# Kernel tuning notes

Measured on AMD Instinct MI355X. Metric: run time of the kernel, lower is better.

## Reference

```python
import jax, jax.numpy as jnp
import numpy as np

EMBED_DIM = 1024
NUM_HEADS = 16
HEAD_DIM = EMBED_DIM // NUM_HEADS


def setup_inputs() -> dict:
    key = jax.random.key(0)
    k_x, k_wqkv, k_bqkv, k_wout, k_bout = jax.random.split(key, 5)
    s = 1.0 / np.sqrt(EMBED_DIM)
    return {
        "x": jax.random.normal(k_x, (2, 2048, EMBED_DIM), dtype=jnp.float32),
        "w_qkv": jax.random.uniform(k_wqkv, (EMBED_DIM, 3 * EMBED_DIM), jnp.float32, -s, s),
        "b_qkv": jax.random.uniform(k_bqkv, (3 * EMBED_DIM,), jnp.float32, -s, s),
        "w_out": jax.random.uniform(k_wout, (EMBED_DIM, EMBED_DIM), jnp.float32, -s, s),
        "b_out": jax.random.uniform(k_bout, (EMBED_DIM,), jnp.float32, -s, s),
    }


def reference(x, w_qkv, b_qkv, w_out, b_out):
    B, S, D = x.shape
    H, Hd = NUM_HEADS, HEAD_DIM
    # qkv projection, then per-head chunk: layout matches torch view(B,S,H,3*Hd).chunk(3,-1)
    qkv = (x @ w_qkv + b_qkv).reshape(B, S, H, 3, Hd)  # [B,S,H,3,Hd]
    q = qkv[..., 0, :]  # [B,S,H,Hd]
    k = qkv[..., 1, :]
    v = qkv[..., 2, :]
    scale = 1.0 / np.sqrt(Hd).astype(np.float32)
    scores = jnp.einsum("bqhd,bkhd->bhqk", q, k) * scale  # [B,H,S,S]
    probs = jax.nn.softmax(scores, axis=-1)
    out = jnp.einsum("bhqk,bkhd->bqhd", probs, v).reshape(B, S, D)
    return out @ w_out + b_out
```

## Files before the change

kernel.cpp:

```cpp
#include <hip/hip_runtime.h>
#include <hip/hip_bf16.h>


typedef __bf16 bf16;
typedef __bf16 bf16x8 __attribute__((ext_vector_type(8)));
typedef float  f32x4  __attribute__((ext_vector_type(4)));
typedef float  f32x16 __attribute__((ext_vector_type(16)));
typedef unsigned int uint;
typedef unsigned int uint2v __attribute__((ext_vector_type(2)));

__device__ __forceinline__ void gload_lds16(const void* g, void* l) {
  __builtin_amdgcn_global_load_lds(
      (const __attribute__((address_space(1))) unsigned int*)g,
      (__attribute__((address_space(3))) unsigned int*)l, 16, 0, 0);
}

__device__ __forceinline__ uint pkbf16(float lo, float hi) {
  union { bf16 h[2]; uint u; } t;
  t.h[0] = (bf16)lo; t.h[1] = (bf16)hi;
  return t.u;
}

__device__ __forceinline__ void pl32swapu(uint& a, uint& b) {
  uint2v r = __builtin_amdgcn_permlane32_swap(a, b, false, false);
  a = r.x; b = r.y;
}
__device__ __forceinline__ void pl32swapf(float& a, float& b) {
  uint ua = __builtin_bit_cast(uint, a), ub = __builtin_bit_cast(uint, b);
  pl32swapu(ua, ub);
  a = __builtin_bit_cast(float, ua); b = __builtin_bit_cast(float, ub);
}

__global__ __launch_bounds__(256) void k_convert(const float* __restrict__ in,
                                                 bf16* __restrict__ out, int n) {
  int i = (blockIdx.x * blockDim.x + threadIdx.x) * 8;
  if (i >= n) return;
  float4 a = *(const float4*)(in + i);
  float4 b = *(const float4*)(in + i + 4);
  bf16x8 o;
  o[0] = (bf16)a.x; o[1] = (bf16)a.y; o[2] = (bf16)a.z; o[3] = (bf16)a.w;
  o[4] = (bf16)b.x; o[5] = (bf16)b.y; o[6] = (bf16)b.z; o[7] = (bf16)b.w;
  *(bf16x8*)(out + i) = o;
}

template<bool PERM>
__global__ __launch_bounds__(256) void k_transpose(const float* __restrict__ in,
                                                   bf16* __restrict__ out, int K, int N) {
  __shared__ float tile[32][33];
  int n0 = blockIdx.x * 32, k0 = blockIdx.y * 32;
  int tx = threadIdx.x, ty = threadIdx.y;
#pragma unroll
  for (int i = 0; i < 4; i++)
    tile[ty + i * 8][tx] = in[(size_t)(k0 + ty + i * 8) * N + n0 + tx];
  __syncthreads();
#pragma unroll
  for (int i = 0; i < 4; i++) {
    int n = n0 + ty + i * 8;
    int row = n;
    if (PERM) {
      int rem = n % 192;
      row = (rem >> 6) * 1024 + (n / 192) * 64 + (rem & 63);
    }
    out[(size_t)row * K + k0 + tx] = (bf16)tile[tx][ty + i * 8];
  }
}

template<int BM, int BN>
__device__ __forceinline__ void gemm_tile(const bf16* __restrict__ A, const bf16* __restrict__ B,
                                          int K, int m0, int n0,
                                          bf16* As, bf16* Bs, f32x4 acc[BM / 32][BN / 32]) {
  const int tid  = threadIdx.x;
  const int lane = tid & 63;
  const int wr   = (tid >> 7) & 1;
  const int wc   = (tid >> 6) & 1;
  constexpr int LA = BM / 64, LB = BN / 64;
  auto stage = [&](int k0v, int b) {
#pragma unroll
    for (int i = 0; i < LA; i++) {
      int row = i * 64 + (tid >> 2);
      int sw  = (tid & 3) ^ (row & 3);
      gload_lds16(A + (size_t)(m0 + row) * K + k0v + sw * 8, (char*)As + b * (BM * 64) + i * 4096 + tid * 16);
    }
#pragma unroll
    for (int i = 0; i < LB; i++) {
      int row = i * 64 + (tid >> 2);
      int sw  = (tid & 3) ^ (row & 3);
      gload_lds16(B + (size_t)(n0 + row) * K + k0v + sw * 8, (char*)Bs + b * (BN * 64) + i * 4096 + tid * 16);
    }
  };
  const int nk = K / 32;
  stage(0, 0); stage(32, 1); stage(64, 2);
  for (int t = 0; t < nk; t++) {
    if (t < nk - 2) {
      if constexpr (LA + LB == 4) asm volatile("s_waitcnt vmcnt(8)" ::: "memory");
      else                        asm volatile("s_waitcnt vmcnt(6)" ::: "memory");
    } else if (t < nk - 1) {
      if constexpr (LA + LB == 4) asm volatile("s_waitcnt vmcnt(4)" ::: "memory");
      else                        asm volatile("s_waitcnt vmcnt(3)" ::: "memory");
    } else {
      asm volatile("s_waitcnt vmcnt(0)" ::: "memory");
    }
    __builtin_amdgcn_s_barrier();
    asm volatile("" ::: "memory");
    if (t + 3 < nk) stage((t + 3) * 32, (t + 3) & 3);
    const int cur = t & 3;
    bf16x8 af[BM / 32], bfr[BN / 32];
#pragma unroll
    for (int r = 0; r < BM / 32; r++) {
      int ra = wr * (BM / 2) + r * 16 + (lane & 15);
      af[r]  = *(const bf16x8*)((const char*)As + cur * (BM * 64) + ra * 64 + ((((lane >> 4) << 4)) ^ ((ra & 3) << 4)));
    }
#pragma unroll
    for (int c = 0; c < BN / 32; c++) {
      int rb = wc * (BN / 2) + c * 16 + (lane & 15);
      bfr[c] = *(const bf16x8*)((const char*)Bs + cur * (BN * 64) + rb * 64 + ((((lane >> 4) << 4)) ^ ((rb & 3) << 4)));
    }
#pragma unroll
    for (int r = 0; r < BM / 32; r++)
#pragma unroll
      for (int c = 0; c < BN / 32; c++)
        acc[r][c] = __builtin_amdgcn_mfma_f32_16x16x32_bf16(af[r], bfr[c], acc[r][c], 0, 0, 0);
    asm volatile("" ::: "memory");
  }
}

__global__ __launch_bounds__(512, 2) void k_gemm_qkv(const bf16* __restrict__ A, const bf16* __restrict__ Bt,
                                                     const float* __restrict__ bias,
                                                     bf16* __restrict__ qb, bf16* __restrict__ kb,
                                                     bf16* __restrict__ vtb) {
  __shared__ char GS[131072];
  const int tid  = threadIdx.x;
  const int lane = tid & 63;
  const int wave = tid >> 6;
  const int wr   = wave >> 2;
  const int wc   = wave & 3;
  const int m0 = blockIdx.x * 256, n0 = blockIdx.y * 256;
  const int K = 1024;

  f32x4 acc[8][4];
  f32x4 zero = {0.f, 0.f, 0.f, 0.f};
#pragma unroll
  for (int ms = 0; ms < 8; ms++)
#pragma unroll
    for (int ns = 0; ns < 4; ns++) acc[ms][ns] = zero;

  const int ccs = tid & 7;
  int rA[2], rB[2];
  {
    int lr0 = tid >> 3;
    rA[0] = lr0;
    rB[0] = (lr0 & 31) + ((lr0 >> 5) << 6);
    int lr1 = 64 + lr0;
    rA[1] = (lr1 & 63) + 128;
    rB[1] = (lr1 & 31) + ((lr1 >> 5) << 6);
  }
  const bf16* Agp[2]; const bf16* Bgp[2];
  int Alo[2], Blo[2];
#pragma unroll
  for (int j = 0; j < 2; j++) {
    Agp[j] = A  + (size_t)(m0 + rA[j]) * K + (ccs ^ (rA[j] & 7)) * 8;
    Alo[j] = rA[j] * 128 + ccs * 16;
    Bgp[j] = Bt + (size_t)(n0 + rB[j]) * K + (ccs ^ (rB[j] & 7)) * 8;
    Blo[j] = rB[j] * 128 + ccs * 16;
  }
  auto stA = [&](int t, int h) {
    int b = t & 1;
#pragma unroll
    for (int j = 0; j < 2; j++)
      gload_lds16(Agp[j] + (size_t)(h * 64) * K + t * 64, GS + b * 32768 + Alo[j] + h * 8192);
  };
  auto stB = [&](int t, int h) {
    int b = t & 1;
#pragma unroll
    for (int j = 0; j < 2; j++)
      gload_lds16(Bgp[j] + (size_t)(h * 32) * K + t * 64, GS + 65536 + b * 32768 + Blo[j] + h * 4096);
  };

  bf16x8 af[4][2], bf0[2][2], bf1[2][2];
  auto rdA = [&](const char* Ab, int mh) {
#pragma unroll
    for (int ms = 0; ms < 4; ms++)
#pragma unroll
      for (int ks = 0; ks < 2; ks++) {
        int row = wr * 128 + (mh * 4 + ms) * 16 + (lane & 15);
        int ch = (ks * 4 + (lane >> 4)) ^ (row & 7);
        af[ms][ks] = *(const bf16x8*)(Ab + row * 128 + ch * 16);
      }
  };
  auto rdB = [&](const char* Bb, int nh, bf16x8 (&bfx)[2][2]) {
#pragma unroll
    for (int ns = 0; ns < 2; ns++)
#pragma unroll
      for (int ks = 0; ks < 2; ks++) {
        int row = wc * 64 + (nh * 2 + ns) * 16 + (lane & 15);
        int ch = (ks * 4 + (lane >> 4)) ^ (row & 7);
        bfx[ns][ks] = *(const bf16x8*)(Bb + row * 128 + ch * 16);
      }
  };
  auto mm = [&](int mh, int nh, bf16x8 (&bfx)[2][2]) {
    __builtin_amdgcn_s_setprio(1);
#pragma unroll
    for (int ks = 0; ks < 2; ks++)
#pragma unroll
      for (int ms = 0; ms < 4; ms++)
#pragma unroll
        for (int ns = 0; ns < 2; ns++)
          acc[mh * 4 + ms][nh * 2 + ns] =
              __builtin_amdgcn_mfma_f32_16x16x32_bf16(af[ms][ks], bfx[ns][ks],
                                                      acc[mh * 4 + ms][nh * 2 + ns], 0, 0, 0);
    __builtin_amdgcn_s_setprio(0);
  };

#define BARRIER do { asm volatile("" ::: "memory"); __builtin_amdgcn_s_barrier(); \
                     asm volatile("" ::: "memory"); } while (0)

  stA(0, 0); stB(0, 0); stB(0, 1); stA(0, 1);
  stA(1, 0); stB(1, 0); stB(1, 1);
  asm volatile("s_waitcnt vmcnt(6)" ::: "memory");
  __builtin_amdgcn_s_barrier();
  asm volatile("" ::: "memory");

  for (int I = 0; I < 8; I++) {
    const int T = 2 * I;
    const char* Ab0 = GS;
    const char* Bb0 = GS + 65536;
    const char* Ab1 = GS + 32768;
    const char* Bb1 = GS + 65536 + 32768;
    const bool m2 = (T + 2 < 16), m3 = (T + 3 < 16);

    rdA(Ab0, 0); rdB(Bb0, 0, bf0);
    stA(T + 1, 1);
    BARRIER;
    mm(0, 0, bf0);

    rdB(Bb0, 1, bf1);
    if (m2) stA(T + 2, 0);
    BARRIER;
    mm(0, 1, bf1);

    rdA(Ab0, 1);
    if (m2) stB(T + 2, 0);
    BARRIER;
    mm(1, 0, bf0);

    if (m2) {
      stB(T + 2, 1);
      asm volatile("s_waitcnt vmcnt(6)" ::: "memory");
    } else {
      asm volatile("s_waitcnt vmcnt(0)" ::: "memory");
    }
    __builtin_amdgcn_s_barrier();
    asm volatile("" ::: "memory");
    mm(1, 1, bf1);

    rdA(Ab1, 0); rdB(Bb1, 0, bf0);
    if (m2) stA(T + 2, 1);
    BARRIER;
    mm(0, 0, bf0);

    rdB(Bb1, 1, bf1);
    if (m3) stA(T + 3, 0);
    BARRIER;
    mm(0, 1, bf1);

    rdA(Ab1, 1);
    if (m3) stB(T + 3, 0);
    BARRIER;
    mm(1, 0, bf0);

    if (m3) {
      stB(T + 3, 1);
      asm volatile("s_waitcnt vmcnt(6)" ::: "memory");
    } else {
      asm volatile("s_waitcnt vmcnt(0)" ::: "memory");
    }
    __builtin_amdgcn_s_barrier();
    asm volatile("" ::: "memory");
    mm(1, 1, bf1);
  }
#undef BARRIER

  const int group = n0 >> 10;
  const int hb = (n0 & 1023) >> 6;
  const int b_ = m0 >> 11;
  const float QSs = 0.125f * 1.4426950408889634f;
  char* TL = GS;

  if (group < 2) {
#pragma unroll
    for (int ms = 0; ms < 8; ms++) {
      int mloc = wr * 128 + ms * 16 + ((lane >> 4) << 2);
#pragma unroll
      for (int ns = 0; ns < 4; ns++) {
        int nloc = wc * 64 + ns * 16 + (lane & 15);
        int np = n0 + nloc;
        float bv = bias[((np & 1023) >> 6) * 192 + group * 64 + (np & 63)];
#pragma unroll
        for (int g = 0; g < 4; g++) {
          float v = acc[ms][ns][g] + bv;
          if (group == 0) v *= QSs;
          int m = mloc + g;
          int byte = m * 512 + ((((nloc >> 3) ^ (m & 7)) << 4) | ((nloc & 7) << 1));
          *(bf16*)(TL + byte) = (bf16)v;
        }
      }
    }
    __syncthreads();
    bf16* dst = (group == 0) ? qb : kb;
#pragma unroll
    for (int it = 0; it < 16; it++) {
      int cid = it * 512 + tid;
      int row = cid >> 5, cc = cid & 31;
      int hh = hb + (cc >> 3), ck = cc & 7;
      bf16x8 v8 = *(const bf16x8*)(TL + row * 512 + ((cc ^ (row & 7)) << 4));
      *(bf16x8*)(dst + ((size_t)(b_ * 16 + hh) * 2048 + (m0 & 2047) + row) * 64 + ck * 8) = v8;
    }
  } else {
#pragma unroll
    for (int ms = 0; ms < 8; ms++) {
      int mloc = wr * 128 + ms * 16 + ((lane >> 4) << 2);
#pragma unroll
      for (int ns = 0; ns < 4; ns++) {
        int nloc = wc * 64 + ns * 16 + (lane & 15);
        int np = n0 + nloc;
        float bv = bias[((np & 1023) >> 6) * 192 + 2 * 64 + (np & 63)];
#pragma unroll
        for (int g = 0; g < 4; g++) {
          float v = acc[ms][ns][g] + bv;
          int m = mloc + g;
          int byte = nloc * 512 + ((((m >> 3) ^ (nloc & 7)) << 4) | ((m & 7) << 1));
          *(bf16*)(TL + byte) = (bf16)v;
        }
      }
    }
    __syncthreads();
#pragma unroll
    for (int it = 0; it < 16; it++) {
      int cid = it * 512 + tid;
      int row = cid >> 5, mc = cid & 31;
      int hh = hb + (row >> 6), dd = row & 63;
      bf16x8 v8 = *(const bf16x8*)(TL + row * 512 + ((mc ^ (row & 7)) << 4));
      *(bf16x8*)(vtb + ((size_t)(b_ * 16 + hh) * 64 + dd) * 2048 + (m0 & 2047) + mc * 8) = v8;
    }
  }
}

__global__ __launch_bounds__(256) void k_gemm_out(const bf16* __restrict__ A, const bf16* __restrict__ Bt,
                                                  const float* __restrict__ bias,
                                                  float* __restrict__ out) {
  __shared__ bf16 As[4 * 64 * 32];
  __shared__ bf16 Bs[4 * 128 * 32];
  int m0 = blockIdx.x * 64, n0 = blockIdx.y * 128;
  f32x4 zero = {0.f, 0.f, 0.f, 0.f};
  f32x4 acc[2][4];
#pragma unroll
  for (int r = 0; r < 2; r++)
#pragma unroll
    for (int c = 0; c < 4; c++) acc[r][c] = zero;
  gemm_tile<64, 128>(A, Bt, 1024, m0, n0, As, Bs, acc);
  const int lane = threadIdx.x & 63;
  const int wr = (threadIdx.x >> 7) & 1, wc = (threadIdx.x >> 6) & 1;
#pragma unroll
  for (int r = 0; r < 2; r++) {
    int mbase = m0 + wr * 32 + r * 16 + ((lane >> 4) << 2);
#pragma unroll
    for (int c = 0; c < 4; c++) {
      int n = n0 + wc * 64 + c * 16 + (lane & 15);
      float bv = bias[n];
#pragma unroll
      for (int g = 0; g < 4; g++)
        out[(size_t)(mbase + g) * 1024 + n] = acc[r][c][g] + bv;
    }
  }
}

__global__ __launch_bounds__(512, 4) void k_attn(const bf16* __restrict__ qb, const bf16* __restrict__ kb,
                                                 const bf16* __restrict__ vtb, bf16* __restrict__ ob) {
  __shared__ char SMEM[73728];
  const int tid  = threadIdx.x;
  const int lane = tid & 63;
  const int wave = tid >> 6;
  const int qsub = wave & 3;
  const int half = wave >> 2;
  const int ln31 = lane & 31;
  const int g    = lane >> 5;

  int l = blockIdx.x;
  int x = l & 7, j = l >> 3;
  int qt = j & 15;
  int bh = x * 4 + (j >> 4);

  const int q0 = qt * 128 + qsub * 32;

  bf16x8 qf[4];
  {
    const bf16* qp = qb + ((size_t)bh * 2048 + q0 + ln31) * 64 + g * 8;
#pragma unroll
    for (int dc = 0; dc < 4; dc++) qf[dc] = *(const bf16x8*)(qp + dc * 16);
  }

  const f32x16 z16 = 0.f;
  f32x16 O0 = 0.f, O1 = 0.f;
  float lacc[4] = {0.f, 0.f, 0.f, 0.f};

  const int rbo = ln31 * 144 + (g << 4);
  const char* kbs0 = SMEM + half * 9216 + rbo;
  const char* kbs1 = SMEM + 36864 + half * 9216 + rbo;
  const char* vbs0 = SMEM + 18432 + half * 9216 + rbo;
  const char* vbs1 = SMEM + 36864 + 18432 + half * 9216 + rbo;

  const int c1 = tid, r1 = c1 / 9, cc1 = c1 % 9;
  const int of1 = (cc1 == 8 ? 0 : cc1) * 8;
  const bf16* kg0a = kb  + ((size_t)bh * 2048 +        r1) * 64 + of1;
  const bf16* kg1a = kb  + ((size_t)bh * 2048 + 1024 + r1) * 64 + of1;
  const bf16* vg0a = vtb + ((size_t)bh * 64 + r1) * 2048 +        of1;
  const bf16* vg1a = vtb + ((size_t)bh * 64 + r1) * 2048 + 1024 + of1;
  const int se = tid >> 6;
  const int ce = 512 + (tid & 63), re = ce / 9, cce = ce % 9;
  const int ofe = (cce == 8 ? 0 : cce) * 8;
  const bf16* gext =
      (se == 0) ? kb  + ((size_t)bh * 2048 +        re) * 64 + ofe :
      (se == 1) ? kb  + ((size_t)bh * 2048 + 1024 + re) * 64 + ofe :
      (se == 2) ? vtb + ((size_t)bh * 64 + re) * 2048 +        ofe :
                  vtb + ((size_t)bh * 64 + re) * 2048 + 1024 + ofe;
  const size_t gadv = (se < 2) ? 4096 : 64;
  const int eoff = se * 9216 + ce * 16;

  auto stage = [&](int t, int s) {
    char* bs = SMEM + s * 36864;
    gload_lds16(kg0a + (size_t)t * 4096, bs +         c1 * 16);
    gload_lds16(kg1a + (size_t)t * 4096, bs + 9216  + c1 * 16);
    gload_lds16(vg0a + t * 64,           bs + 18432 + c1 * 16);
    gload_lds16(vg1a + t * 64,           bs + 27648 + c1 * 16);
    if (tid < 256) gload_lds16(gext + (size_t)t * gadv, bs + eoff);
  };

  auto smx = [&](f32x16& sv, bf16x8& f0, bf16x8& f1) {
#pragma unroll
    for (int r = 0; r < 16; r++) sv[r] = __builtin_amdgcn_exp2f(sv[r]);
#pragma unroll
    for (int r = 0; r < 4; r++)
      lacc[r] += (sv[r] + sv[r + 4]) + (sv[r + 8] + sv[r + 12]);
    uint a0 = pkbf16(sv[0], sv[1]), a1 = pkbf16(sv[2], sv[3]);
    uint a2 = pkbf16(sv[4], sv[5]), a3 = pkbf16(sv[6], sv[7]);
    pl32swapu(a0, a2); pl32swapu(a1, a3);
    union { uint w[4]; bf16x8 v; } pa;
    pa.w[0] = a0; pa.w[1] = a1; pa.w[2] = a2; pa.w[3] = a3;
    f0 = pa.v;
    uint b0 = pkbf16(sv[8], sv[9]),  b1 = pkbf16(sv[10], sv[11]);
    uint b2 = pkbf16(sv[12], sv[13]), b3 = pkbf16(sv[14], sv[15]);
    pl32swapu(b0, b2); pl32swapu(b1, b3);
    union { uint w[4]; bf16x8 v; } pb;
    pb.w[0] = b0; pb.w[1] = b1; pb.w[2] = b2; pb.w[3] = b3;
    f1 = pb.v;
  };

  stage(0, 0);
  for (int t = 0; t < 16; t++) {
    asm volatile("s_waitcnt vmcnt(0)" ::: "memory");
    __builtin_amdgcn_s_barrier();
    asm volatile("" ::: "memory");
    if (t + 1 < 16) stage(t + 1, (t + 1) & 1);

    const char* Kb = (t & 1) ? kbs1 : kbs0;
    const char* Vb = (t & 1) ? vbs1 : vbs0;

    f32x16 sA, sB;
    __builtin_amdgcn_s_setprio(1);
    sA = __builtin_amdgcn_mfma_f32_32x32x16_bf16(*(const bf16x8*)(Kb +    0), qf[0], z16, 0, 0, 0);
    sB = __builtin_amdgcn_mfma_f32_32x32x16_bf16(*(const bf16x8*)(Kb + 4608), qf[0], z16, 0, 0, 0);
#pragma unroll
    for (int dc = 1; dc < 4; dc++) {
      sA = __builtin_amdgcn_mfma_f32_32x32x16_bf16(*(const bf16x8*)(Kb + dc * 32),        qf[dc], sA, 0, 0, 0);
      sB = __builtin_amdgcn_mfma_f32_32x32x16_bf16(*(const bf16x8*)(Kb + 4608 + dc * 32), qf[dc], sB, 0, 0, 0);
    }
    __builtin_amdgcn_s_setprio(0);

    bf16x8 fA0, fA1, fB0, fB1;
    smx(sA, fA0, fA1);
    __builtin_amdgcn_s_setprio(1);
    O0 = __builtin_amdgcn_mfma_f32_32x32x16_bf16(*(const bf16x8*)(Vb +    0), fA0, O0, 0, 0, 0);
    O1 = __builtin_amdgcn_mfma_f32_32x32x16_bf16(*(const bf16x8*)(Vb + 4608), fA0, O1, 0, 0, 0);
    O0 = __builtin_amdgcn_mfma_f32_32x32x16_bf16(*(const bf16x8*)(Vb +   32), fA1, O0, 0, 0, 0);
    O1 = __builtin_amdgcn_mfma_f32_32x32x16_bf16(*(const bf16x8*)(Vb + 4640), fA1, O1, 0, 0, 0);
    __builtin_amdgcn_s_setprio(0);
    smx(sB, fB0, fB1);
    __builtin_amdgcn_s_setprio(1);
    O0 = __builtin_amdgcn_mfma_f32_32x32x16_bf16(*(const bf16x8*)(Vb +   64), fB0, O0, 0, 0, 0);
    O1 = __builtin_amdgcn_mfma_f32_32x32x16_bf16(*(const bf16x8*)(Vb + 4672), fB0, O1, 0, 0, 0);
    O0 = __builtin_amdgcn_mfma_f32_32x32x16_bf16(*(const bf16x8*)(Vb +   96), fB1, O0, 0, 0, 0);
    O1 = __builtin_amdgcn_mfma_f32_32x32x16_bf16(*(const bf16x8*)(Vb + 4704), fB1, O1, 0, 0, 0);
    __builtin_amdgcn_s_setprio(0);
    asm volatile("" ::: "memory");
  }

  float l_r = (lacc[0] + lacc[1]) + (lacc[2] + lacc[3]);
  { float o = l_r; pl32swapf(l_r, o); l_r += o; }

  float* Opart = (float*)SMEM;
  float* Ls    = (float*)(SMEM + 36864);
  __syncthreads();
  if (half == 1) {
    float* my = Opart + (qsub * 64 + lane) * 36;
#pragma unroll
    for (int c = 0; c < 4; c++) {
      f32x4 a = {O0[c * 4], O0[c * 4 + 1], O0[c * 4 + 2], O0[c * 4 + 3]};
      f32x4 b = {O1[c * 4], O1[c * 4 + 1], O1[c * 4 + 2], O1[c * 4 + 3]};
      *(f32x4*)(my + c * 4) = a;
      *(f32x4*)(my + 16 + c * 4) = b;
    }
    if (lane < 32) Ls[qsub * 32 + ln31] = l_r;
  }
  __syncthreads();
  bf16 (*Os)[32][72] = reinterpret_cast<bf16 (*)[32][72]>(SMEM + 40960);
  if (half == 0) {
    const float* pr = Opart + (qsub * 64 + lane) * 36;
#pragma unroll
    for (int c = 0; c < 4; c++) {
      f32x4 a = *(const f32x4*)(pr + c * 4);
      f32x4 b = *(const f32x4*)(pr + 16 + c * 4);
#pragma unroll
      for (int k = 0; k < 4; k++) { O0[c * 4 + k] += a[k]; O1[c * 4 + k] += b[k]; }
    }
    l_r += Ls[qsub * 32 + ln31];
    float inv = 1.0f / l_r;
#pragma unroll
    for (int r = 0; r < 16; r++) {
      int d0 = (r & 3) + 8 * (r >> 2) + 4 * g;
      Os[qsub][ln31][d0]      = (bf16)(O0[r] * inv);
      Os[qsub][ln31][d0 + 32] = (bf16)(O1[r] * inv);
    }
  }
  __syncthreads();
  if (half == 0) {
    int b_ = bh >> 4, h = bh & 15;
#pragma unroll
    for (int it = 0; it < 4; it++) {
      int cid = it * 64 + lane;
      int row = cid >> 3, c = cid & 7;
      bf16x8 v8o = *(const bf16x8*)&Os[qsub][row][c * 8];
      *(bf16x8*)(ob + ((size_t)(b_ * 2048 + q0 + row)) * 1024 + h * 64 + c * 8) = v8o;
    }
  }
}

extern "C" void kernel_launch(void* const* d_in, const int* in_sizes, int n_in,
                              void* d_out, int out_size, void* d_ws, size_t ws_size,
                              hipStream_t stream) {
  const float* x     = (const float*)d_in[0];
  const float* w_qkv = (const float*)d_in[1];
  const float* b_qkv = (const float*)d_in[2];
  const float* w_out = (const float*)d_in[3];
  const float* b_out = (const float*)d_in[4];
  float* out = (float*)d_out;

  char* ws = (char*)d_ws;
  bf16* xb  = (bf16*)ws;
  bf16* wqT = (bf16*)(ws + (8ull  << 20));
  bf16* woT = (bf16*)(ws + (14ull << 20));
  bf16* qb  = (bf16*)(ws + (16ull << 20));
  bf16* kb  = (bf16*)(ws + (24ull << 20));
  bf16* vtb = (bf16*)(ws + (32ull << 20));

  k_convert<<<2048, 256, 0, stream>>>(x, xb, 4194304);
  k_transpose<true><<<dim3(96, 32), dim3(32, 8), 0, stream>>>(w_qkv, wqT, 1024, 3072);
  k_transpose<false><<<dim3(32, 32), dim3(32, 8), 0, stream>>>(w_out, woT, 1024, 1024);
  k_gemm_qkv<<<dim3(16, 12), 512, 0, stream>>>(xb, wqT, b_qkv, qb, kb, vtb);
  k_attn<<<512, 512, 0, stream>>>(qb, kb, vtb, xb);
  k_gemm_out<<<dim3(64, 8), 256, 0, stream>>>(xb, woT, b_out, out);
}
```

Measured before the change: 112.4 us.

## Process two 32-row query tiles per wave in attention and fuse prep kernels

The attention kernel now gives each wave 64 query rows (two 32-row MFMA tiles) instead of 32. Each K and V fragment read from LDS is reused across both tiles, and the grid halves to 256 blocks. The three preprocessing kernels (x conversion and two weight transposes) are merged into one launch to cut launch overhead. The cost is more accumulator registers (launch bound lowered to 2 blocks per SM) and fewer blocks, which may leave compute units idle on a 256-CU device.

```diff
diff --git a/kernel.cpp b/kernel.cpp
--- a/kernel.cpp
+++ b/kernel.cpp
@@ -31,24 +31,34 @@
   a = __builtin_bit_cast(float, ua); b = __builtin_bit_cast(float, ub);
 }
 
-__global__ __launch_bounds__(256) void k_convert(const float* __restrict__ in,
-                                                 bf16* __restrict__ out, int n) {
-  int i = (blockIdx.x * blockDim.x + threadIdx.x) * 8;
-  if (i >= n) return;
-  float4 a = *(const float4*)(in + i);
-  float4 b = *(const float4*)(in + i + 4);
-  bf16x8 o;
-  o[0] = (bf16)a.x; o[1] = (bf16)a.y; o[2] = (bf16)a.z; o[3] = (bf16)a.w;
-  o[4] = (bf16)b.x; o[5] = (bf16)b.y; o[6] = (bf16)b.z; o[7] = (bf16)b.w;
-  *(bf16x8*)(out + i) = o;
-}
-
-template<bool PERM>
-__global__ __launch_bounds__(256) void k_transpose(const float* __restrict__ in,
-                                                   bf16* __restrict__ out, int K, int N) {
+__global__ __launch_bounds__(256) void k_prep(const float* __restrict__ x,
+                                              const float* __restrict__ w_qkv,
+                                              const float* __restrict__ w_out,
+                                              bf16* __restrict__ xb,
+                                              bf16* __restrict__ wqT,
+                                              bf16* __restrict__ woT) {
   __shared__ float tile[32][33];
-  int n0 = blockIdx.x * 32, k0 = blockIdx.y * 32;
-  int tx = threadIdx.x, ty = threadIdx.y;
+  const int b = blockIdx.x;
+  const int tid = threadIdx.x;
+  if (b < 2048) {
+    int i = (b * 256 + tid) * 8;
+    float4 a = *(const float4*)(x + i);
+    float4 c = *(const float4*)(x + i + 4);
+    bf16x8 o;
+    o[0] = (bf16)a.x; o[1] = (bf16)a.y; o[2] = (bf16)a.z; o[3] = (bf16)a.w;
+    o[4] = (bf16)c.x; o[5] = (bf16)c.y; o[6] = (bf16)c.z; o[7] = (bf16)c.w;
+    *(bf16x8*)(xb + i) = o;
+    return;
+  }
+  const bool perm = (b < 5120);
+  const float* in = perm ? w_qkv : w_out;
+  bf16* out = perm ? wqT : woT;
+  const int N = perm ? 3072 : 1024;
+  int idx = perm ? (b - 2048) : (b - 5120);
+  int gx = perm ? (idx % 96) : (idx % 32);
+  int gy = perm ? (idx / 96) : (idx / 32);
+  int n0 = gx * 32, k0 = gy * 32;
+  int tx = tid & 31, ty = tid >> 5;
 #pragma unroll
   for (int i = 0; i < 4; i++)
     tile[ty + i * 8][tx] = in[(size_t)(k0 + ty + i * 8) * N + n0 + tx];
@@ -57,11 +67,11 @@
   for (int i = 0; i < 4; i++) {
     int n = n0 + ty + i * 8;
     int row = n;
-    if (PERM) {
+    if (perm) {
       int rem = n % 192;
       row = (rem >> 6) * 1024 + (n / 192) * 64 + (rem & 63);
     }
-    out[(size_t)row * K + k0 + tx] = (bf16)tile[tx][ty + i * 8];
+    out[(size_t)row * 1024 + k0 + tx] = (bf16)tile[tx][ty + i * 8];
   }
 }
 
@@ -374,34 +384,39 @@
   }
 }
 
-__global__ __launch_bounds__(512, 4) void k_attn(const bf16* __restrict__ qb, const bf16* __restrict__ kb,
+__global__ __launch_bounds__(512, 2) void k_attn(const bf16* __restrict__ qb, const bf16* __restrict__ kb,
                                                  const bf16* __restrict__ vtb, bf16* __restrict__ ob) {
   __shared__ char SMEM[73728];
   const int tid  = threadIdx.x;
   const int lane = tid & 63;
   const int wave = tid >> 6;
-  const int qsub = wave & 3;
+  const int qp   = wave & 3;
   const int half = wave >> 2;
   const int ln31 = lane & 31;
   const int g    = lane >> 5;
 
   int l = blockIdx.x;
   int x = l & 7, j = l >> 3;
-  int qt = j & 15;
-  int bh = x * 4 + (j >> 4);
-
-  const int q0 = qt * 128 + qsub * 32;
-
-  bf16x8 qf[4];
+  int qt = j & 7;
+  int bh = x * 4 + (j >> 3);
+
+  const int q0 = qt * 256 + qp * 64;
+
+  bf16x8 qfa[4], qfb[4];
   {
-    const bf16* qp = qb + ((size_t)bh * 2048 + q0 + ln31) * 64 + g * 8;
-#pragma unroll
-    for (int dc = 0; dc < 4; dc++) qf[dc] = *(const bf16x8*)(qp + dc * 16);
+    const bf16* qpa = qb + ((size_t)bh * 2048 + q0 + ln31) * 64 + g * 8;
+    const bf16* qpb = qb + ((size_t)bh * 2048 + q0 + 32 + ln31) * 64 + g * 8;
+#pragma unroll
+    for (int dc = 0; dc < 4; dc++) {
+      qfa[dc] = *(const bf16x8*)(qpa + dc * 16);
+      qfb[dc] = *(const bf16x8*)(qpb + dc * 16);
+    }
   }
 
   const f32x16 z16 = 0.f;
-  f32x16 O0 = 0.f, O1 = 0.f;
-  float lacc[4] = {0.f, 0.f, 0.f, 0.f};
+  f32x16 Oa0 = 0.f, Oa1 = 0.f, Ob0 = 0.f, Ob1 = 0.f;
+  float lacc_a[4] = {0.f, 0.f, 0.f, 0.f};
+  float lacc_b[4] = {0.f, 0.f, 0.f, 0.f};
 
   const int rbo = ln31 * 144 + (g << 4);
   const char* kbs0 = SMEM + half * 9216 + rbo;
@@ -435,12 +450,12 @@
     if (tid < 256) gload_lds16(gext + (size_t)t * gadv, bs + eoff);
   };
 
-  auto smx = [&](f32x16& sv, bf16x8& f0, bf16x8& f1) {
+  auto smx = [&](f32x16& sv, bf16x8& f0, bf16x8& f1, float (&lc)[4]) {
 #pragma unroll
     for (int r = 0; r < 16; r++) sv[r] = __builtin_amdgcn_exp2f(sv[r]);
 #pragma unroll
     for (int r = 0; r < 4; r++)
-      lacc[r] += (sv[r] + sv[r + 4]) + (sv[r + 8] + sv[r + 12]);
+      lc[r] += (sv[r] + sv[r + 4]) + (sv[r + 8] + sv[r + 12]);
     uint a0 = pkbf16(sv[0], sv[1]), a1 = pkbf16(sv[2], sv[3]);
     uint a2 = pkbf16(sv[4], sv[5]), a3 = pkbf16(sv[6], sv[7]);
     pl32swapu(a0, a2); pl32swapu(a1, a3);
@@ -465,81 +480,128 @@
     const char* Kb = (t & 1) ? kbs1 : kbs0;
     const char* Vb = (t & 1) ? vbs1 : vbs0;
 
-    f32x16 sA, sB;
+    f32x16 sAa, sAb, sBa, sBb;
     __builtin_amdgcn_s_setprio(1);
-    sA = __builtin_amdgcn_mfma_f32_32x32x16_bf16(*(const bf16x8*)(Kb +    0), qf[0], z16, 0, 0, 0);
-    sB = __builtin_amdgcn_mfma_f32_32x32x16_bf16(*(const bf16x8*)(Kb + 4608), qf[0], z16, 0, 0, 0);
+    {
+      bf16x8 kA = *(const bf16x8*)(Kb + 0);
+      bf16x8 kB = *(const bf16x8*)(Kb + 4608);
+      sAa = __builtin_amdgcn_mfma_f32_32x32x16_bf16(kA, qfa[0], z16, 0, 0, 0);
+      sAb = __builtin_amdgcn_mfma_f32_32x32x16_bf16(kA, qfb[0], z16, 0, 0, 0);
+      sBa = __builtin_amdgcn_mfma_f32_32x32x16_bf16(kB, qfa[0], z16, 0, 0, 0);
+      sBb = __builtin_amdgcn_mfma_f32_32x32x16_bf16(kB, qfb[0], z16, 0, 0, 0);
+    }
 #pragma unroll
     for (int dc = 1; dc < 4; dc++) {
-      sA = __builtin_amdgcn_mfma_f32_32x32x16_bf16(*(const bf16x8*)(Kb + dc * 32),        qf[dc], sA, 0, 0, 0);
-      sB = __builtin_amdgcn_mfma_f32_32x32x16_bf16(*(const bf16x8*)(Kb + 4608 + dc * 32), qf[dc], sB, 0, 0, 0);
+      bf16x8 kA = *(const bf16x8*)(Kb + dc * 32);
+      bf16x8 kB = *(const bf16x8*)(Kb + 4608 + dc * 32);
+      sAa = __builtin_amdgcn_mfma_f32_32x32x16_bf16(kA, qfa[dc], sAa, 0, 0, 0);
+      sAb = __builtin_amdgcn_mfma_f32_32x32x16_bf16(kA, qfb[dc], sAb, 0, 0, 0);
+      sBa = __builtin_amdgcn_mfma_f32_32x32x16_bf16(kB, qfa[dc], sBa, 0, 0, 0);
+      sBb = __builtin_amdgcn_mfma_f32_32x32x16_bf16(kB, qfb[dc], sBb, 0, 0, 0);
     }
     __builtin_amdgcn_s_setprio(0);
 
-    bf16x8 fA0, fA1, fB0, fB1;
-    smx(sA, fA0, fA1);
+    bf16x8 fa0, fa1, fb0, fb1;
+    smx(sAa, fa0, fa1, lacc_a);
+    smx(sAb, fb0, fb1, lacc_b);
     __builtin_amdgcn_s_setprio(1);
-    O0 = __builtin_amdgcn_mfma_f32_32x32x16_bf16(*(const bf16x8*)(Vb +    0), fA0, O0, 0, 0, 0);
-    O1 = __builtin_amdgcn_mfma_f32_32x32x16_bf16(*(const bf16x8*)(Vb + 4608), fA0, O1, 0, 0, 0);
-    O0 = __builtin_amdgcn_mfma_f32_32x32x16_bf16(*(const bf16x8*)(Vb +   32), fA1, O0, 0, 0, 0);
-    O1 = __builtin_amdgcn_mfma_f32_32x32x16_bf16(*(const bf16x8*)(Vb + 4640), fA1, O1, 0, 0, 0);
+    {
+      bf16x8 v0 = *(const bf16x8*)(Vb + 0);
+      bf16x8 v1 = *(const bf16x8*)(Vb + 4608);
+      Oa0 = __builtin_amdgcn_mfma_f32_32x32x16_bf16(v0, fa0, Oa0, 0, 0, 0);
+      Ob0 = __builtin_amdgcn_mfma_f32_32x32x16_bf16(v0, fb0, Ob0, 0, 0, 0);
+      Oa1 = __builtin_amdgcn_mfma_f32_32x32x16_bf16(v1, fa0, Oa1, 0, 0, 0);
+      Ob1 = __builtin_amdgcn_mfma_f32_32x32x16_bf16(v1, fb0, Ob1, 0, 0, 0);
+      v0 = *(const bf16x8*)(Vb + 32);
+      v1 = *(const bf16x8*)(Vb + 4640);
+      Oa0 = __builtin_amdgcn_mfma_f32_32x32x16_bf16(v0, fa1, Oa0, 0, 0, 0);
+      Ob0 = __builtin_amdgcn_mfma_f32_32x32x16_bf16(v0, fb1, Ob0, 0, 0, 0);
+      Oa1 = __builtin_amdgcn_mfma_f32_32x32x16_bf16(v1, fa1, Oa1, 0, 0, 0);
+      Ob1 = __builtin_amdgcn_mfma_f32_32x32x16_bf16(v1, fb1, Ob1, 0, 0, 0);
+    }
     __builtin_amdgcn_s_setprio(0);
-    smx(sB, fB0, fB1);
+    smx(sBa, fa0, fa1, lacc_a);
+    smx(sBb, fb0, fb1, lacc_b);
     __builtin_amdgcn_s_setprio(1);
-    O0 = __builtin_amdgcn_mfma_f32_32x32x16_bf16(*(const bf16x8*)(Vb +   64), fB0, O0, 0, 0, 0);
-    O1 = __builtin_amdgcn_mfma_f32_32x32x16_bf16(*(const bf16x8*)(Vb + 4672), fB0, O1, 0, 0, 0);
-    O0 = __builtin_amdgcn_mfma_f32_32x32x16_bf16(*(const bf16x8*)(Vb +   96), fB1, O0, 0, 0, 0);
-    O1 = __builtin_amdgcn_mfma_f32_32x32x16_bf16(*(const bf16x8*)(Vb + 4704), fB1, O1, 0, 0, 0);
+    {
+      bf16x8 v0 = *(const bf16x8*)(Vb + 64);
+      bf16x8 v1 = *(const bf16x8*)(Vb + 4672);
+      Oa0 = __builtin_amdgcn_mfma_f32_32x32x16_bf16(v0, fa0, Oa0, 0, 0, 0);
+      Ob0 = __builtin_amdgcn_mfma_f32_32x32x16_bf16(v0, fb0, Ob0, 0, 0, 0);
+      Oa1 = __builtin_amdgcn_mfma_f32_32x32x16_bf16(v1, fa0, Oa1, 0, 0, 0);
+      Ob1 = __builtin_amdgcn_mfma_f32_32x32x16_bf16(v1, fb0, Ob1, 0, 0, 0);
+      v0 = *(const bf16x8*)(Vb + 96);
+      v1 = *(const bf16x8*)(Vb + 4704);
+      Oa0 = __builtin_amdgcn_mfma_f32_32x32x16_bf16(v0, fa1, Oa0, 0, 0, 0);
+      Ob0 = __builtin_amdgcn_mfma_f32_32x32x16_bf16(v0, fb1, Ob0, 0, 0, 0);
+      Oa1 = __builtin_amdgcn_mfma_f32_32x32x16_bf16(v1, fa1, Oa1, 0, 0, 0);
+      Ob1 = __builtin_amdgcn_mfma_f32_32x32x16_bf16(v1, fb1, Ob1, 0, 0, 0);
+    }
     __builtin_amdgcn_s_setprio(0);
     asm volatile("" ::: "memory");
   }
 
-  float l_r = (lacc[0] + lacc[1]) + (lacc[2] + lacc[3]);
-  { float o = l_r; pl32swapf(l_r, o); l_r += o; }
+  float l_ra = (lacc_a[0] + lacc_a[1]) + (lacc_a[2] + lacc_a[3]);
+  { float o = l_ra; pl32swapf(l_ra, o); l_ra += o; }
+  float l_rb = (lacc_b[0] + lacc_b[1]) + (lacc_b[2] + lacc_b[3]);
+  { float o = l_rb; pl32swapf(l_rb, o); l_rb += o; }
 
   float* Opart = (float*)SMEM;
-  float* Ls    = (float*)(SMEM + 36864);
+  float* LsA   = (float*)(SMEM + 69632);
+  float* LsB   = (float*)(SMEM + 70144);
   __syncthreads();
   if (half == 1) {
-    float* my = Opart + (qsub * 64 + lane) * 36;
+    float* my = Opart + (qp * 64 + lane) * 68;
 #pragma unroll
     for (int c = 0; c < 4; c++) {
-      f32x4 a = {O0[c * 4], O0[c * 4 + 1], O0[c * 4 + 2], O0[c * 4 + 3]};
-      f32x4 b = {O1[c * 4], O1[c * 4 + 1], O1[c * 4 + 2], O1[c * 4 + 3]};
-      *(f32x4*)(my + c * 4) = a;
-      *(f32x4*)(my + 16 + c * 4) = b;
-    }
-    if (lane < 32) Ls[qsub * 32 + ln31] = l_r;
+      *(f32x4*)(my +      c * 4) = f32x4{Oa0[c*4], Oa0[c*4+1], Oa0[c*4+2], Oa0[c*4+3]};
+      *(f32x4*)(my + 16 + c * 4) = f32x4{Oa1[c*4], Oa1[c*4+1], Oa1[c*4+2], Oa1[c*4+3]};
+      *(f32x4*)(my + 32 + c * 4) = f32x4{Ob0[c*4], Ob0[c*4+1], Ob0[c*4+2], Ob0[c*4+3]};
+      *(f32x4*)(my + 48 + c * 4) = f32x4{Ob1[c*4], Ob1[c*4+1], Ob1[c*4+2], Ob1[c*4+3]};
+    }
+    if (lane < 32) { LsA[qp * 32 + ln31] = l_ra; LsB[qp * 32 + ln31] = l_rb; }
   }
   __syncthreads();
-  bf16 (*Os)[32][72] = reinterpret_cast<bf16 (*)[32][72]>(SMEM + 40960);
+  float inva = 0.f, invb = 0.f;
   if (half == 0) {
-    const float* pr = Opart + (qsub * 64 + lane) * 36;
+    const float* pr = Opart + (qp * 64 + lane) * 68;
 #pragma unroll
     for (int c = 0; c < 4; c++) {
-      f32x4 a = *(const f32x4*)(pr + c * 4);
-      f32x4 b = *(const f32x4*)(pr + 16 + c * 4);
-#pragma unroll
-      for (int k = 0; k < 4; k++) { O0[c * 4 + k] += a[k]; O1[c * 4 + k] += b[k]; }
-    }
-    l_r += Ls[qsub * 32 + ln31];
-    float inv = 1.0f / l_r;
+      f32x4 a0 = *(const f32x4*)(pr +      c * 4);
+      f32x4 a1 = *(const f32x4*)(pr + 16 + c * 4);
+      f32x4 b0 = *(const f32x4*)(pr + 32 + c * 4);
+      f32x4 b1 = *(const f32x4*)(pr + 48 + c * 4);
+#pragma unroll
+      for (int k = 0; k < 4; k++) {
+        Oa0[c*4+k] += a0[k]; Oa1[c*4+k] += a1[k];
+        Ob0[c*4+k] += b0[k]; Ob1[c*4+k] += b1[k];
+      }
+    }
+    inva = 1.0f / (l_ra + LsA[qp * 32 + ln31]);
+    invb = 1.0f / (l_rb + LsB[qp * 32 + ln31]);
+  }
+  __syncthreads();
+  bf16 (*Os)[64][72] = reinterpret_cast<bf16 (*)[64][72]>(SMEM);
+  if (half == 0) {
 #pragma unroll
     for (int r = 0; r < 16; r++) {
       int d0 = (r & 3) + 8 * (r >> 2) + 4 * g;
-      Os[qsub][ln31][d0]      = (bf16)(O0[r] * inv);
-      Os[qsub][ln31][d0 + 32] = (bf16)(O1[r] * inv);
+      Os[qp][ln31][d0]           = (bf16)(Oa0[r] * inva);
+      Os[qp][ln31][d0 + 32]      = (bf16)(Oa1[r] * inva);
+      Os[qp][32 + ln31][d0]      = (bf16)(Ob0[r] * invb);
+      Os[qp][32 + ln31][d0 + 32] = (bf16)(Ob1[r] * invb);
     }
   }
   __syncthreads();
-  if (half == 0) {
+  {
     int b_ = bh >> 4, h = bh & 15;
 #pragma unroll
     for (int it = 0; it < 4; it++) {
-      int cid = it * 64 + lane;
-      int row = cid >> 3, c = cid & 7;
-      bf16x8 v8o = *(const bf16x8*)&Os[qsub][row][c * 8];
-      *(bf16x8*)(ob + ((size_t)(b_ * 2048 + q0 + row)) * 1024 + h * 64 + c * 8) = v8o;
+      int cid = it * 512 + tid;
+      int row256 = cid >> 3, c = cid & 7;
+      int qpp = row256 >> 6, row = row256 & 63;
+      bf16x8 v8o = *(const bf16x8*)&Os[qpp][row][c * 8];
+      *(bf16x8*)(ob + ((size_t)(b_ * 2048 + qt * 256 + qpp * 64 + row)) * 1024 + h * 64 + c * 8) = v8o;
     }
   }
 }
@@ -562,10 +624,8 @@
   bf16* kb  = (bf16*)(ws + (24ull << 20));
   bf16* vtb = (bf16*)(ws + (32ull << 20));
 
-  k_convert<<<2048, 256, 0, stream>>>(x, xb, 4194304);
-  k_transpose<true><<<dim3(96, 32), dim3(32, 8), 0, stream>>>(w_qkv, wqT, 1024, 3072);
-  k_transpose<false><<<dim3(32, 32), dim3(32, 8), 0, stream>>>(w_out, woT, 1024, 1024);
+  k_prep<<<6144, 256, 0, stream>>>(x, w_qkv, w_out, xb, wqT, woT);
   k_gemm_qkv<<<dim3(16, 12), 512, 0, stream>>>(xb, wqT, b_qkv, qb, kb, vtb);
-  k_attn<<<512, 512, 0, stream>>>(qb, kb, vtb, xb);
+  k_attn<<<256, 512, 0, stream>>>(qb, kb, vtb, xb);
   k_gemm_out<<<dim3(64, 8), 256, 0, stream>>>(xb, woT, b_out, out);
 }
```

Measured after the change: 103.9 us. -7.6%, faster.
